# Performance work log

Hardware: AMD Instinct MI355X
Metric: run time of the kernel (lower is better)

Reference implementation:

```python
import jax, jax.numpy as jnp
import numpy as np

N_NODES = 100000
NUM_FEATURES = 512
HIDDEN = 128
OUT = 2
N_EDGES = 1600000


def setup_inputs() -> dict:
    key = jax.random.key(0)
    k_x, k_e, k_w1, k_b1, k_w2, k_b2 = jax.random.split(key, 6)
    x = jax.random.normal(k_x, (N_NODES, NUM_FEATURES), dtype=jnp.float32)
    edge_index = jax.random.randint(k_e, (2, N_EDGES), 0, N_NODES, dtype=jnp.int64)
    # GCNConv weight (Glorot-style scale) and bias
    w1 = jax.random.normal(k_w1, (NUM_FEATURES, HIDDEN), dtype=jnp.float32) / np.sqrt(NUM_FEATURES)
    b1 = jnp.zeros((HIDDEN,), dtype=jnp.float32)
    # nn.Linear weight/bias
    w2 = jax.random.normal(k_w2, (HIDDEN, OUT), dtype=jnp.float32) / np.sqrt(HIDDEN)
    b2 = jnp.zeros((OUT,), dtype=jnp.float32)
    return {"x": x, "w1": w1, "b1": b1, "w2": w2, "b2": b2, "edge_index": edge_index}


def _gcn_conv(x, edge_index, w, b, num_nodes):
    """PyG GCNConv: h = D^{-1/2} (A+I) D^{-1/2} (x @ w) + b."""
    h = x @ w  # [N, hidden] -- transform before propagate (PyG order)
    loops = jnp.arange(num_nodes, dtype=edge_index.dtype)
    src = jnp.concatenate([edge_index[0], loops])  # [E+N]
    dst = jnp.concatenate([edge_index[1], loops])
    # symmetric normalization: deg computed over destination (col) incl. self-loops
    deg = jnp.zeros((num_nodes,), dtype=h.dtype).at[dst].add(1.0)
    dinv = jax.lax.rsqrt(deg)  # deg >= 1 thanks to self-loops
    norm = dinv[src] * dinv[dst]  # [E+N]
    msg = h[src] * norm[:, None]  # gather + scale, [E+N, hidden]
    out = jax.ops.segment_sum(msg, dst, num_segments=num_nodes)  # scatter-add
    return out + b


def reference(x, w1, b1, w2, b2, edge_index):
    h = _gcn_conv(x, edge_index, w1, b1, N_NODES)  # [N, hidden]
    return h @ w2 + b2  # [N, out]
```

## Files before the change

### kernel.cpp

```cpp
#include <hip/hip_runtime.h>

constexpr int N_NODES = 100000;
constexpr int N_FEAT  = 512;
constexpr int N_EDGES = 1600000;

constexpr float FXS = 1048576.0f;
constexpr float FXB = 32.0f;

constexpr int BSH    = 8;
constexpr int BINW   = 1 << BSH;
constexpr int NBINS  = (N_NODES + BINW - 1) >> BSH;
constexpr int NSH    = 8;
constexpr int BCAP_S = 768;
constexpr int NBB    = 500;
constexpr int CHUNK  = N_EDGES / NBB;
constexpr int GRID   = 2048;
constexpr int NRB    = GRID - NBB;
constexpr int NCUR   = NBINS * NSH;

constexpr int TROWS  = 16;
constexpr int NTILE  = N_NODES / TROWS;
constexpr int TSPLIT = NTILE - NRB * 4;
static_assert(TSPLIT >= 0 && TSPLIT < NRB, "tile split");
constexpr int SCR_STRIDE = 136;

typedef float vfloat4 __attribute__((ext_vector_type(4)));

constexpr int WS_W    = 0;
constexpr int WS_C    = 1024;
constexpr int WS_CUR  = 1056;
constexpr int WS_DEG  = WS_CUR + 3200;
constexpr int WS_DINV = WS_DEG + N_NODES;
constexpr int WS_G    = WS_DINV + N_NODES;
constexpr int WS_FXP  = WS_G + 2 * N_NODES;
constexpr int WS_BINS = WS_FXP + 2 * N_NODES;

static_assert((WS_G * 4) % 8 == 0, "g alignment");
static_assert((WS_FXP * 4) % 8 == 0, "fxp alignment");

__global__ void k_prep(const float* __restrict__ w1, const float* __restrict__ w2,
                       const float* __restrict__ b1, const float* __restrict__ b2,
                       float* __restrict__ ws) {
    int i = blockIdx.x * blockDim.x + threadIdx.x;
    if (i < NCUR) reinterpret_cast<int*>(ws + WS_CUR)[i] = 0;
    if (i < N_FEAT) {
        float a0 = 0.f, a1 = 0.f;
        for (int m = 0; m < 128; ++m) {
            float w = w1[i * 128 + m];
            a0 += w * w2[m * 2 + 0];
            a1 += w * w2[m * 2 + 1];
        }
        ws[WS_W + i] = a0;
        ws[WS_W + 512 + i] = a1;
        if (i < 2) {
            float s = b2[i];
            for (int m = 0; m < 128; ++m) s += b1[m] * w2[m * 2 + i];
            ws[WS_C + i] = s;
        }
    }
}

__global__ __launch_bounds__(256) void k_fused(
    const float* __restrict__ x, float* __restrict__ ws,
    const int* __restrict__ src, const int* __restrict__ dst,
    float2* __restrict__ g) {
    int b = blockIdx.x;
    int tid = threadIdx.x;

    __shared__ __align__(16) char smem[2 * TROWS * SCR_STRIDE * 4];

    if (b < NBB) {
        int* cnt  = reinterpret_cast<int*>(smem);
        int* offs = cnt + NBINS;
        int* cur2 = offs + NBINS;
        int sg = b & (NSH - 1);
        for (int i = tid; i < NBINS; i += 256) { cnt[i] = 0; cur2[i] = 0; }
        __syncthreads();
        int base = b * CHUNK;
        for (int e = base + tid; e < base + CHUNK; e += 256)
            atomicAdd(&cnt[dst[e] >> BSH], 1);
        __syncthreads();
        int* gcur = reinterpret_cast<int*>(ws + WS_CUR);
        for (int i = tid; i < NBINS; i += 256) {
            int c = cnt[i];
            int pos = c ? atomicAdd(&gcur[i * NSH + sg], c) : 0;
            offs[i] = (i * NSH + sg) * BCAP_S + pos;
        }
        __syncthreads();
        unsigned int* bins = reinterpret_cast<unsigned int*>(ws + WS_BINS);
        for (int e = base + tid; e < base + CHUNK; e += 256) {
            int d = dst[e], s = src[e];
            int bin = d >> BSH;
            int r = atomicAdd(&cur2[bin], 1);
            bins[offs[bin] + r] = (unsigned int)s | ((unsigned int)(d & (BINW - 1)) << 17);
        }
        return;
    }

    float (*scrA)[SCR_STRIDE] = reinterpret_cast<float (*)[SCR_STRIDE]>(smem);
    float (*scrB)[SCR_STRIDE] =
        reinterpret_cast<float (*)[SCR_STRIDE]>(smem + TROWS * SCR_STRIDE * 4);

    int rb = b - NBB;
    int t0, tcnt;
    if (rb < TSPLIT) { t0 = rb * 5;                     tcnt = 5; }
    else             { t0 = TSPLIT * 5 + (rb - TSPLIT) * 4; tcnt = 4; }

    int c = tid & 127;
    int row_lo = tid >> 7;
    const vfloat4* Wq = reinterpret_cast<const vfloat4*>(ws + WS_W);
    vfloat4 w0c = Wq[c];
    vfloat4 w1c = Wq[128 + c];

    int lane16 = tid & 15;
    int rrow   = tid >> 4;

    for (int tt = t0; tt < t0 + tcnt; ++tt) {
        int r0 = tt * TROWS;
        const vfloat4* xq = reinterpret_cast<const vfloat4*>(x) + (size_t)r0 * 128;
        vfloat4 xv[8];
        #pragma unroll
        for (int i = 0; i < 8; ++i)
            xv[i] = xq[i * 256 + tid];
        #pragma unroll
        for (int i = 0; i < 8; ++i) {
            float pa = xv[i].x*w0c.x + xv[i].y*w0c.y + xv[i].z*w0c.z + xv[i].w*w0c.w;
            float pb = xv[i].x*w1c.x + xv[i].y*w1c.y + xv[i].z*w1c.z + xv[i].w*w1c.w;
            scrA[2 * i + row_lo][c] = pa;
            scrB[2 * i + row_lo][c] = pb;
        }
        __syncthreads();
        const float4* rA = reinterpret_cast<const float4*>(&scrA[rrow][0]);
        const float4* rB = reinterpret_cast<const float4*>(&scrB[rrow][0]);
        float4 aq0 = rA[lane16 * 2], aq1 = rA[lane16 * 2 + 1];
        float4 bq0 = rB[lane16 * 2], bq1 = rB[lane16 * 2 + 1];
        float sa = aq0.x + aq0.y + aq0.z + aq0.w + aq1.x + aq1.y + aq1.z + aq1.w;
        float sb = bq0.x + bq0.y + bq0.z + bq0.w + bq1.x + bq1.y + bq1.z + bq1.w;
        #pragma unroll
        for (int off = 1; off <= 8; off <<= 1) {
            sa += __shfl_xor(sa, off);
            sb += __shfl_xor(sb, off);
        }
        if (lane16 == 0) g[r0 + rrow] = make_float2(sa, sb);
        __syncthreads();
    }
}

__global__ __launch_bounds__(512) void k_deg(float* __restrict__ ws) {
    int b = blockIdx.x;
    int tid = threadIdx.x;
    const int* gcur = reinterpret_cast<const int*>(ws + WS_CUR);
    const unsigned int* bins = reinterpret_cast<const unsigned int*>(ws + WS_BINS);
    __shared__ int cnt[BINW];
    if (tid < BINW) cnt[tid] = 0;
    __syncthreads();
    #pragma unroll
    for (int sg = 0; sg < NSH; ++sg) {
        int cell = b * NSH + sg;
        int n = min(gcur[cell], BCAP_S);
        const unsigned int* bb = bins + (size_t)cell * BCAP_S;
        for (int i = tid; i < n; i += 512)
            atomicAdd(&cnt[bb[i] >> 17], 1);
    }
    __syncthreads();
    int d = (b << BSH) + tid;
    if (tid < BINW && d < N_NODES) {
        int dg = cnt[tid] + 1;
        reinterpret_cast<int*>(ws + WS_DEG)[d] = dg;
        float di = rsqrtf((float)dg);
        ws[WS_DINV + d] = di;
        float2 gv = reinterpret_cast<const float2*>(ws + WS_G)[d];
        unsigned int lo = (unsigned int)__float2int_rn((gv.x * di + FXB) * FXS);
        unsigned int hi = (unsigned int)__float2int_rn((gv.y * di + FXB) * FXS);
        reinterpret_cast<unsigned long long*>(ws + WS_FXP)[d] =
            ((unsigned long long)hi << 32) | (unsigned long long)lo;
    }
}

__global__ __launch_bounds__(512) void k_pass2(float* __restrict__ ws,
                                               float2* __restrict__ out) {
    int b = blockIdx.x;
    int tid = threadIdx.x;
    const int* gcur = reinterpret_cast<const int*>(ws + WS_CUR);
    const unsigned int* bins = reinterpret_cast<const unsigned int*>(ws + WS_BINS);
    const int* deg = reinterpret_cast<const int*>(ws + WS_DEG);
    const float* dinv = ws + WS_DINV;
    const unsigned long long* fxp = reinterpret_cast<const unsigned long long*>(ws + WS_FXP);
    __shared__ unsigned long long acc[BINW];
    if (tid < BINW) acc[tid] = 0ull;
    __syncthreads();
    #pragma unroll
    for (int sg = 0; sg < NSH; ++sg) {
        int cell = b * NSH + sg;
        int n = min(gcur[cell], BCAP_S);
        const unsigned int* bb = bins + (size_t)cell * BCAP_S;
        int i = tid;
        for (; i + 512 < n; i += 1024) {
            unsigned int p0 = bb[i], p1 = bb[i + 512];
            unsigned long long v0 = fxp[p0 & 0x1FFFFu];
            unsigned long long v1 = fxp[p1 & 0x1FFFFu];
            atomicAdd(&acc[p0 >> 17], v0);
            atomicAdd(&acc[p1 >> 17], v1);
        }
        if (i < n) {
            unsigned int p = bb[i];
            atomicAdd(&acc[p >> 17], fxp[p & 0x1FFFFu]);
        }
    }
    __syncthreads();
    int d = (b << BSH) + tid;
    if (tid < BINW && d < N_NODES) {
        unsigned long long a = acc[tid] + fxp[d];
        long long dg = (long long)deg[d];
        long long bias = dg << 25;
        long long lo = (long long)(a & 0xFFFFFFFFull) - bias;
        long long hi = (long long)(a >> 32) - bias;
        float di = dinv[d];
        out[d] = make_float2(di * ((float)lo * (1.0f / FXS)) + ws[WS_C + 0],
                             di * ((float)hi * (1.0f / FXS)) + ws[WS_C + 1]);
    }
}

extern "C" void kernel_launch(void* const* d_in, const int* in_sizes, int n_in,
                              void* d_out, int out_size, void* d_ws, size_t ws_size,
                              hipStream_t stream) {
    const float* x  = (const float*)d_in[0];
    const float* w1 = (const float*)d_in[1];
    const float* b1 = (const float*)d_in[2];
    const float* w2 = (const float*)d_in[3];
    const float* b2 = (const float*)d_in[4];
    const int*   ei = (const int*)d_in[5];
    float* ws = (float*)d_ws;

    float2* g = (float2*)(ws + WS_G);

    k_prep<<<13, 256, 0, stream>>>(w1, w2, b1, b2, ws);
    k_fused<<<GRID, 256, 0, stream>>>(x, ws, ei, ei + N_EDGES, g);
    k_deg<<<NBINS, 512, 0, stream>>>(ws);
    k_pass2<<<NBINS, 512, 0, stream>>>(ws, (float2*)d_out);
}
```

Before: 77.70 us.

## Split fused binning/row-dot kernel into separate launches with more bin blocks

The fused kernel that divided its grid between edge-binning blocks and x·W row-dot blocks becomes two kernels: k_bin with twice as many blocks (smaller edge chunks, dst cached in shared memory so it is read only once) and k_rowdot over 2048 blocks handling 3-4 tiles each. This is meant to fix load imbalance between the two roles and cut a redundant dst read. It adds an extra launch and serializes the two phases instead of letting them run concurrently.

```diff
diff --git a/kernel.cpp b/kernel.cpp
--- a/kernel.cpp
+++ b/kernel.cpp
@@ -12,16 +12,15 @@
 constexpr int NBINS  = (N_NODES + BINW - 1) >> BSH;
 constexpr int NSH    = 8;
 constexpr int BCAP_S = 768;
-constexpr int NBB    = 500;
+constexpr int NBB    = 1000;
 constexpr int CHUNK  = N_EDGES / NBB;
-constexpr int GRID   = 2048;
-constexpr int NRB    = GRID - NBB;
 constexpr int NCUR   = NBINS * NSH;
 
-constexpr int TROWS  = 16;
-constexpr int NTILE  = N_NODES / TROWS;
-constexpr int TSPLIT = NTILE - NRB * 4;
-static_assert(TSPLIT >= 0 && TSPLIT < NRB, "tile split");
+constexpr int GRID_RD = 2048;
+constexpr int TROWS   = 16;
+constexpr int NTILE   = N_NODES / TROWS;
+constexpr int T4      = NTILE - GRID_RD * 3;
+static_assert(T4 >= 0 && T4 < GRID_RD, "tile split");
 constexpr int SCR_STRIDE = 136;
 
 typedef float vfloat4 __attribute__((ext_vector_type(4)));
@@ -60,51 +59,51 @@
     }
 }
 
-__global__ __launch_bounds__(256) void k_fused(
-    const float* __restrict__ x, float* __restrict__ ws,
-    const int* __restrict__ src, const int* __restrict__ dst,
+__global__ __launch_bounds__(256) void k_bin(
+    float* __restrict__ ws, const int* __restrict__ src, const int* __restrict__ dst) {
+    int b = blockIdx.x;
+    int tid = threadIdx.x;
+    __shared__ int cnt[NBINS];
+    __shared__ int offs[NBINS];
+    __shared__ int cur2[NBINS];
+    __shared__ int dstl[CHUNK];
+    int sg = b & (NSH - 1);
+    for (int i = tid; i < NBINS; i += 256) { cnt[i] = 0; cur2[i] = 0; }
+    __syncthreads();
+    int base = b * CHUNK;
+    for (int e = tid; e < CHUNK; e += 256) {
+        int d = dst[base + e];
+        dstl[e] = d;
+        atomicAdd(&cnt[d >> BSH], 1);
+    }
+    __syncthreads();
+    int* gcur = reinterpret_cast<int*>(ws + WS_CUR);
+    for (int i = tid; i < NBINS; i += 256) {
+        int c = cnt[i];
+        int pos = c ? atomicAdd(&gcur[i * NSH + sg], c) : 0;
+        offs[i] = (i * NSH + sg) * BCAP_S + pos;
+    }
+    __syncthreads();
+    unsigned int* bins = reinterpret_cast<unsigned int*>(ws + WS_BINS);
+    for (int e = tid; e < CHUNK; e += 256) {
+        int d = dstl[e], s = src[base + e];
+        int bin = d >> BSH;
+        int r = atomicAdd(&cur2[bin], 1);
+        bins[offs[bin] + r] = (unsigned int)s | ((unsigned int)(d & (BINW - 1)) << 17);
+    }
+}
+
+__global__ __launch_bounds__(256) void k_rowdot(
+    const float* __restrict__ x, const float* __restrict__ ws,
     float2* __restrict__ g) {
     int b = blockIdx.x;
     int tid = threadIdx.x;
-
-    __shared__ __align__(16) char smem[2 * TROWS * SCR_STRIDE * 4];
-
-    if (b < NBB) {
-        int* cnt  = reinterpret_cast<int*>(smem);
-        int* offs = cnt + NBINS;
-        int* cur2 = offs + NBINS;
-        int sg = b & (NSH - 1);
-        for (int i = tid; i < NBINS; i += 256) { cnt[i] = 0; cur2[i] = 0; }
-        __syncthreads();
-        int base = b * CHUNK;
-        for (int e = base + tid; e < base + CHUNK; e += 256)
-            atomicAdd(&cnt[dst[e] >> BSH], 1);
-        __syncthreads();
-        int* gcur = reinterpret_cast<int*>(ws + WS_CUR);
-        for (int i = tid; i < NBINS; i += 256) {
-            int c = cnt[i];
-            int pos = c ? atomicAdd(&gcur[i * NSH + sg], c) : 0;
-            offs[i] = (i * NSH + sg) * BCAP_S + pos;
-        }
-        __syncthreads();
-        unsigned int* bins = reinterpret_cast<unsigned int*>(ws + WS_BINS);
-        for (int e = base + tid; e < base + CHUNK; e += 256) {
-            int d = dst[e], s = src[e];
-            int bin = d >> BSH;
-            int r = atomicAdd(&cur2[bin], 1);
-            bins[offs[bin] + r] = (unsigned int)s | ((unsigned int)(d & (BINW - 1)) << 17);
-        }
-        return;
-    }
-
-    float (*scrA)[SCR_STRIDE] = reinterpret_cast<float (*)[SCR_STRIDE]>(smem);
-    float (*scrB)[SCR_STRIDE] =
-        reinterpret_cast<float (*)[SCR_STRIDE]>(smem + TROWS * SCR_STRIDE * 4);
-
-    int rb = b - NBB;
+    __shared__ __align__(16) float scrA[TROWS][SCR_STRIDE];
+    __shared__ __align__(16) float scrB[TROWS][SCR_STRIDE];
+
     int t0, tcnt;
-    if (rb < TSPLIT) { t0 = rb * 5;                     tcnt = 5; }
-    else             { t0 = TSPLIT * 5 + (rb - TSPLIT) * 4; tcnt = 4; }
+    if (b < T4) { t0 = b * 4;              tcnt = 4; }
+    else        { t0 = T4 * 4 + (b - T4) * 3; tcnt = 3; }
 
     int c = tid & 127;
     int row_lo = tid >> 7;
@@ -235,7 +234,8 @@
     float2* g = (float2*)(ws + WS_G);
 
     k_prep<<<13, 256, 0, stream>>>(w1, w2, b1, b2, ws);
-    k_fused<<<GRID, 256, 0, stream>>>(x, ws, ei, ei + N_EDGES, g);
+    k_bin<<<NBB, 256, 0, stream>>>(ws, ei, ei + N_EDGES);
+    k_rowdot<<<GRID_RD, 256, 0, stream>>>(x, ws, g);
     k_deg<<<NBINS, 512, 0, stream>>>(ws);
     k_pass2<<<NBINS, 512, 0, stream>>>(ws, (float2*)d_out);
 }
```

Result: slower. 105.9 us (+36.3%).
